# Optimization experiments

Hardware: AMD Instinct MI355X
Metric: run time of the kernel (lower is better)

The kernel has to match this reference:

```python
import jax, jax.numpy as jnp
import numpy as np

N, F, D, H = 8192, 128, 128, 2
LEAKY_ALPHA = 0.3  # keras.layers.LeakyReLU default


def setup_inputs() -> dict:
    key = jax.random.key(0)
    ks = jax.random.split(key, 8)
    x = jax.random.normal(ks[0], (N, F), dtype=jnp.float32)
    # sparse-ish binary adjacency with self loops, stored dense (as the module does)
    adj = (jax.random.uniform(ks[1], (N, N)) < 0.01).astype(jnp.float32)
    adj = jnp.clip(adj + jnp.eye(N, dtype=jnp.float32), 0.0, 1.0)
    s = 1.0 / np.sqrt(F)
    Wmap = jax.random.normal(ks[2], (H, F, D), dtype=jnp.float32) * s
    a1_w = jax.random.normal(ks[3], (H, D), dtype=jnp.float32) * (1.0 / np.sqrt(D))
    a2_w = jax.random.normal(ks[4], (H, D), dtype=jnp.float32) * (1.0 / np.sqrt(D))
    a1_b = jnp.zeros((H,), dtype=jnp.float32)
    a2_b = jnp.zeros((H,), dtype=jnp.float32)
    kernel = jax.random.normal(ks[5], (H, F, D), dtype=jnp.float32) * s
    bias = jnp.zeros((H, N, D), dtype=jnp.float32)
    return {"x": x, "adj": adj, "Wmap": Wmap, "a1_w": a1_w, "a1_b": a1_b,
            "a2_w": a2_w, "a2_b": a2_b, "kernel": kernel, "bias": bias}


def reference(x, adj, Wmap, a1_w, a1_b, a2_w, a2_b, kernel, bias):
    # per-head Conv1D(k=1, no bias): node-wise linear map  [H, N, D]
    mapped = jnp.einsum('nf,hfd->hnd', x, Wmap)
    # per-head Conv1D(k=1) scalar scores  [H, N]
    sa1 = jnp.einsum('hnd,hd->hn', mapped, a1_w) + a1_b[:, None]
    sa2 = jnp.einsum('hnd,hd->hn', mapped, a2_w) + a2_b[:, None]
    # additive score masked multiplicatively by adjacency:  [H, N, N]
    w = adj[None, :, :] * sa1[:, :, None] + adj[None, :, :] * sa2[:, None, :]
    w = jnp.where(w >= 0, w, LEAKY_ALPHA * w)
    att = jax.nn.softmax(w, axis=-1)  # softmax over neighbors (incl. zeroed entries, as in source)
    value = jnp.einsum('nf,hfd->hnd', x, kernel)
    out = jnp.einsum('hnm,hmd->hnd', att, value) + bias  # [H, N, D]
    return out.mean(axis=0)  # attn_heads_reduction='average', linear activation
```

## Files before the change

### kernel.cpp

```cpp
#include <hip/hip_runtime.h>
#include <hip/hip_bf16.h>

#define NN 8192
#define FF 128
#define DD 128
#define HH 2
#define ALPHA 0.3f
#define MAXNNZ 1024

__global__ __launch_bounds__(256) void c_kernel(
    const float* __restrict__ Wmap, const float* __restrict__ a1w,
    const float* __restrict__ a2w, float* __restrict__ c1, float* __restrict__ c2) {
  int t = threadIdx.x;
  int h = t >> 7, f = t & 127;
  const float* wrow = Wmap + ((size_t)h * FF + f) * DD;
  const float* a1 = a1w + h * DD;
  const float* a2 = a2w + h * DD;
  float s1 = 0.f, s2 = 0.f;
  #pragma unroll 8
  for (int d = 0; d < DD; d++) {
    float w = wrow[d];
    s1 += w * a1[d];
    s2 += w * a2[d];
  }
  c1[t] = s1;
  c2[t] = s2;
}

__global__ __launch_bounds__(128) void sa_kernel(
    const float* __restrict__ x, const float* __restrict__ c1,
    const float* __restrict__ c2, const float* __restrict__ a1b,
    const float* __restrict__ a2b, float* __restrict__ sa1, float* __restrict__ sa2) {
  int n = blockIdx.x;
  int f = threadIdx.x;
  float xv = x[(size_t)n * FF + f];
  float p00 = xv * c1[f];
  float p01 = xv * c1[FF + f];
  float p10 = xv * c2[f];
  float p11 = xv * c2[FF + f];
  #pragma unroll
  for (int o = 32; o > 0; o >>= 1) {
    p00 += __shfl_down(p00, o);
    p01 += __shfl_down(p01, o);
    p10 += __shfl_down(p10, o);
    p11 += __shfl_down(p11, o);
  }
  __shared__ float part[2][4];
  int w = f >> 6;
  if ((f & 63) == 0) {
    part[w][0] = p00; part[w][1] = p01; part[w][2] = p10; part[w][3] = p11;
  }
  __syncthreads();
  if (f == 0) {
    sa1[n]      = part[0][0] + part[1][0] + a1b[0];
    sa1[NN + n] = part[0][1] + part[1][1] + a1b[1];
    sa2[n]      = part[0][2] + part[1][2] + a2b[0];
    sa2[NN + n] = part[0][3] + part[1][3] + a2b[1];
  }
}

__global__ __launch_bounds__(256) void value_gemm(
    const float* __restrict__ x, const float* __restrict__ kern,
    float* __restrict__ value) {
  int h = blockIdx.y;
  int row0 = blockIdx.x * 32;
  __shared__ float Bl[64 * 128];
  __shared__ float Al[32 * 129];
  const float4* Bg4 = (const float4*)(kern + (size_t)h * FF * DD);
  const float4* Ag4 = (const float4*)(x + (size_t)row0 * FF);
  float4* Bl4 = (float4*)Bl;
  int tid = threadIdx.x;

  #pragma unroll
  for (int q = 0; q < 4; q++) {
    int idx = q * 256 + tid;
    int r = idx >> 5, c4 = idx & 31;
    float4 g = Ag4[idx];
    Al[r * 129 + c4 * 4 + 0] = g.x;
    Al[r * 129 + c4 * 4 + 1] = g.y;
    Al[r * 129 + c4 * 4 + 2] = g.z;
    Al[r * 129 + c4 * 4 + 3] = g.w;
  }

  int cg = tid & 31;
  int rg = tid >> 5;
  float4 acc[4];
  #pragma unroll
  for (int m = 0; m < 4; m++) acc[m] = make_float4(0.f, 0.f, 0.f, 0.f);

  for (int kp = 0; kp < 2; kp++) {
    __syncthreads();
    #pragma unroll
    for (int q = 0; q < 8; q++)
      Bl4[q * 256 + tid] = Bg4[kp * 2048 + q * 256 + tid];
    __syncthreads();
    for (int k2 = 0; k2 < 64; k2++) {
      int k = kp * 64 + k2;
      float4 bv = *(const float4*)&Bl[k2 * 128 + cg * 4];
      #pragma unroll
      for (int m = 0; m < 4; m++) {
        float av = Al[(rg + m * 8) * 129 + k];
        acc[m].x += av * bv.x;
        acc[m].y += av * bv.y;
        acc[m].z += av * bv.z;
        acc[m].w += av * bv.w;
      }
    }
  }
  #pragma unroll
  for (int m = 0; m < 4; m++) {
    int r = row0 + rg + m * 8;
    *(float4*)&value[((size_t)h * NN + r) * DD + cg * 4] = acc[m];
  }
}

__global__ __launch_bounds__(128) void colsum_kernel(
    const float* __restrict__ value, float* __restrict__ colsum) {
  int h = blockIdx.y, chunk = blockIdx.x, d = threadIdx.x;
  const float* v = value + ((size_t)h * NN + (size_t)chunk * 128) * DD;
  float s = 0.f;
  #pragma unroll 4
  for (int r = 0; r < 128; r++) s += v[r * DD + d];
  atomicAdd(&colsum[h * DD + d], s);
}

__global__ __launch_bounds__(256) void gat_main(
    const float* __restrict__ adj, const float* __restrict__ sa1,
    const float* __restrict__ sa2, const float* __restrict__ value,
    const float* __restrict__ colsum, const float* __restrict__ bias,
    float* __restrict__ out) {
  int i = blockIdx.x;
  __shared__ int idxbuf[MAXNNZ];
  __shared__ float em1buf[HH][MAXNNZ];
  __shared__ int cnt;
  __shared__ float sume_sh[HH];
  __shared__ float wred[4][HH];
  __shared__ float contrib[256];
  int t = threadIdx.x;
  if (t == 0) cnt = 0;
  __syncthreads();

  const float4* arow = (const float4*)(adj + (size_t)i * NN);
  #pragma unroll
  for (int q = 0; q < 8; q++) {
    int f4 = q * 256 + t;
    float4 a = arow[f4];
    int j0 = f4 * 4;
    if (a.x != 0.f) { int p = atomicAdd(&cnt, 1); if (p < MAXNNZ) idxbuf[p] = j0; }
    if (a.y != 0.f) { int p = atomicAdd(&cnt, 1); if (p < MAXNNZ) idxbuf[p] = j0 + 1; }
    if (a.z != 0.f) { int p = atomicAdd(&cnt, 1); if (p < MAXNNZ) idxbuf[p] = j0 + 2; }
    if (a.w != 0.f) { int p = atomicAdd(&cnt, 1); if (p < MAXNNZ) idxbuf[p] = j0 + 3; }
  }
  __syncthreads();
  int count = min(cnt, MAXNNZ);

  float s10 = sa1[i];
  float s11 = sa1[NN + i];
  float l0 = 0.f, l1 = 0.f;
  for (int k = t; k < count; k += 256) {
    int j = idxbuf[k];
    float w0 = s10 + sa2[j];
    float w1 = s11 + sa2[NN + j];
    w0 = (w0 >= 0.f) ? w0 : ALPHA * w0;
    w1 = (w1 >= 0.f) ? w1 : ALPHA * w1;
    float e0 = __expf(w0) - 1.f;
    float e1 = __expf(w1) - 1.f;
    em1buf[0][k] = e0;
    em1buf[1][k] = e1;
    l0 += e0;
    l1 += e1;
  }
  #pragma unroll
  for (int o = 32; o > 0; o >>= 1) {
    l0 += __shfl_down(l0, o);
    l1 += __shfl_down(l1, o);
  }
  int wid = t >> 6;
  if ((t & 63) == 0) { wred[wid][0] = l0; wred[wid][1] = l1; }
  __syncthreads();
  if (t == 0) {
    sume_sh[0] = wred[0][0] + wred[1][0] + wred[2][0] + wred[3][0];
    sume_sh[1] = wred[0][1] + wred[1][1] + wred[2][1] + wred[3][1];
  }
  __syncthreads();

  int h = t >> 7, d = t & 127;
  const float* val = value + (size_t)h * NN * DD + d;
  const float* eb = em1buf[h];
  float acc = 0.f;
  #pragma unroll 4
  for (int k = 0; k < count; k++) {
    int j = idxbuf[k];
    acc += eb[k] * val[(size_t)j * DD];
  }
  float denom = (float)NN + sume_sh[h];
  float r = (colsum[h * DD + d] + acc) / denom +
            bias[((size_t)h * NN + i) * DD + d];
  contrib[t] = r;
  __syncthreads();
  if (t < 128) out[(size_t)i * DD + t] = 0.5f * (contrib[t] + contrib[t + 128]);
}

extern "C" void kernel_launch(void* const* d_in, const int* in_sizes, int n_in,
                              void* d_out, int out_size, void* d_ws, size_t ws_size,
                              hipStream_t stream) {
  const float* x    = (const float*)d_in[0];
  const float* adj  = (const float*)d_in[1];
  const float* Wmap = (const float*)d_in[2];
  const float* a1w  = (const float*)d_in[3];
  const float* a1b  = (const float*)d_in[4];
  const float* a2w  = (const float*)d_in[5];
  const float* a2b  = (const float*)d_in[6];
  const float* kern = (const float*)d_in[7];
  const float* bias = (const float*)d_in[8];
  float* out = (float*)d_out;
  float* ws  = (float*)d_ws;

  float* c1     = ws;
  float* c2     = ws + 256;
  float* sa1    = ws + 512;
  float* sa2    = ws + 16896;
  float* colsum = ws + 33280;
  float* value  = ws + 33536;

  hipMemsetAsync(colsum, 0, HH * DD * sizeof(float), stream);
  c_kernel<<<1, 256, 0, stream>>>(Wmap, a1w, a2w, c1, c2);
  sa_kernel<<<NN, 128, 0, stream>>>(x, c1, c2, a1b, a2b, sa1, sa2);
  value_gemm<<<dim3(NN / 32, HH), 256, 0, stream>>>(x, kern, value);
  colsum_kernel<<<dim3(NN / 128, HH), 128, 0, stream>>>(value, colsum);
  gat_main<<<NN, 256, 0, stream>>>(adj, sa1, sa2, value, colsum, bias, out);
}
```

Measured before the change: 455.4 us.

## Store value in bf16, fuse colsum into GEMM, wave-aggregate neighbor compaction

The value matrix is now stored as bf16, which halves the bytes of the gathered neighbor rows read in the main attention kernel. The column-sum kernel is removed and its work folded into the GEMM epilogue through a shared-memory reduction and atomics. Neighbor index compaction uses one wave-level ballot plus a single atomic per wave instead of one atomic per nonzero. The output store is vectorized to float2. bf16 values lower the accuracy of the weighted sum, while colsum is still accumulated from the fp32 results.

After: 468.1 us. +2.8%, slower.

```diff
diff --git a/kernel.cpp b/kernel.cpp
--- a/kernel.cpp
+++ b/kernel.cpp
@@ -61,7 +61,7 @@
 
 __global__ __launch_bounds__(256) void value_gemm(
     const float* __restrict__ x, const float* __restrict__ kern,
-    float* __restrict__ value) {
+    unsigned short* __restrict__ value_bf, float* __restrict__ colsum) {
   int h = blockIdx.y;
   int row0 = blockIdx.x * 32;
   __shared__ float Bl[64 * 128];
@@ -107,26 +107,46 @@
       }
     }
   }
+
   #pragma unroll
   for (int m = 0; m < 4; m++) {
     int r = row0 + rg + m * 8;
-    *(float4*)&value[((size_t)h * NN + r) * DD + cg * 4] = acc[m];
-  }
-}
-
-__global__ __launch_bounds__(128) void colsum_kernel(
-    const float* __restrict__ value, float* __restrict__ colsum) {
-  int h = blockIdx.y, chunk = blockIdx.x, d = threadIdx.x;
-  const float* v = value + ((size_t)h * NN + (size_t)chunk * 128) * DD;
-  float s = 0.f;
-  #pragma unroll 4
-  for (int r = 0; r < 128; r++) s += v[r * DD + d];
-  atomicAdd(&colsum[h * DD + d], s);
+    ushort4 pk;
+    __hip_bfloat16 b0 = __float2bfloat16(acc[m].x);
+    __hip_bfloat16 b1 = __float2bfloat16(acc[m].y);
+    __hip_bfloat16 b2 = __float2bfloat16(acc[m].z);
+    __hip_bfloat16 b3 = __float2bfloat16(acc[m].w);
+    pk.x = *(unsigned short*)&b0;
+    pk.y = *(unsigned short*)&b1;
+    pk.z = *(unsigned short*)&b2;
+    pk.w = *(unsigned short*)&b3;
+    *(ushort4*)&value_bf[((size_t)h * NN + r) * DD + cg * 4] = pk;
+  }
+
+  float4 cp;
+  cp.x = acc[0].x + acc[1].x + acc[2].x + acc[3].x;
+  cp.y = acc[0].y + acc[1].y + acc[2].y + acc[3].y;
+  cp.z = acc[0].z + acc[1].z + acc[2].z + acc[3].z;
+  cp.w = acc[0].w + acc[1].w + acc[2].w + acc[3].w;
+  __syncthreads();
+  float* colred = Al;
+  *(float4*)&colred[rg * 128 + cg * 4] = cp;
+  __syncthreads();
+  if (rg == 0) {
+    #pragma unroll
+    for (int c = 0; c < 4; c++) {
+      int col = cg * 4 + c;
+      float s = 0.f;
+      #pragma unroll
+      for (int rr = 0; rr < 8; rr++) s += colred[rr * 128 + col];
+      atomicAdd(&colsum[h * DD + col], s);
+    }
+  }
 }
 
 __global__ __launch_bounds__(256) void gat_main(
     const float* __restrict__ adj, const float* __restrict__ sa1,
-    const float* __restrict__ sa2, const float* __restrict__ value,
+    const float* __restrict__ sa2, const unsigned short* __restrict__ value_bf,
     const float* __restrict__ colsum, const float* __restrict__ bias,
     float* __restrict__ out) {
   int i = blockIdx.x;
@@ -137,6 +157,7 @@
   __shared__ float wred[4][HH];
   __shared__ float contrib[256];
   int t = threadIdx.x;
+  int lane = t & 63;
   if (t == 0) cnt = 0;
   __syncthreads();
 
@@ -146,10 +167,20 @@
     int f4 = q * 256 + t;
     float4 a = arow[f4];
     int j0 = f4 * 4;
-    if (a.x != 0.f) { int p = atomicAdd(&cnt, 1); if (p < MAXNNZ) idxbuf[p] = j0; }
-    if (a.y != 0.f) { int p = atomicAdd(&cnt, 1); if (p < MAXNNZ) idxbuf[p] = j0 + 1; }
-    if (a.z != 0.f) { int p = atomicAdd(&cnt, 1); if (p < MAXNNZ) idxbuf[p] = j0 + 2; }
-    if (a.w != 0.f) { int p = atomicAdd(&cnt, 1); if (p < MAXNNZ) idxbuf[p] = j0 + 3; }
+    float av[4] = {a.x, a.y, a.z, a.w};
+    #pragma unroll
+    for (int c = 0; c < 4; c++) {
+      bool nz = (av[c] != 0.f);
+      unsigned long long m = __ballot(nz);
+      int tot = __popcll(m);
+      int base = 0;
+      if (lane == 0 && tot) base = atomicAdd(&cnt, tot);
+      base = __shfl(base, 0);
+      if (nz) {
+        int p = base + __popcll(m & ((1ull << lane) - 1ull));
+        if (p < MAXNNZ) idxbuf[p] = j0 + c;
+      }
+    }
   }
   __syncthreads();
   int count = min(cnt, MAXNNZ);
@@ -176,7 +207,7 @@
     l1 += __shfl_down(l1, o);
   }
   int wid = t >> 6;
-  if ((t & 63) == 0) { wred[wid][0] = l0; wred[wid][1] = l1; }
+  if (lane == 0) { wred[wid][0] = l0; wred[wid][1] = l1; }
   __syncthreads();
   if (t == 0) {
     sume_sh[0] = wred[0][0] + wred[1][0] + wred[2][0] + wred[3][0];
@@ -185,20 +216,27 @@
   __syncthreads();
 
   int h = t >> 7, d = t & 127;
-  const float* val = value + (size_t)h * NN * DD + d;
+  const unsigned short* val = value_bf + (size_t)h * NN * DD + d;
   const float* eb = em1buf[h];
   float acc = 0.f;
   #pragma unroll 4
   for (int k = 0; k < count; k++) {
     int j = idxbuf[k];
-    acc += eb[k] * val[(size_t)j * DD];
+    unsigned short u = val[(size_t)j * DD];
+    __hip_bfloat16 bv = *(__hip_bfloat16*)&u;
+    acc += eb[k] * __bfloat162float(bv);
   }
   float denom = (float)NN + sume_sh[h];
   float r = (colsum[h * DD + d] + acc) / denom +
             bias[((size_t)h * NN + i) * DD + d];
   contrib[t] = r;
   __syncthreads();
-  if (t < 128) out[(size_t)i * DD + t] = 0.5f * (contrib[t] + contrib[t + 128]);
+  if (t < 64) {
+    float2 o2;
+    o2.x = 0.5f * (contrib[2 * t]     + contrib[2 * t + 128]);
+    o2.y = 0.5f * (contrib[2 * t + 1] + contrib[2 * t + 129]);
+    *(float2*)&out[(size_t)i * DD + 2 * t] = o2;
+  }
 }
 
 extern "C" void kernel_launch(void* const* d_in, const int* in_sizes, int n_in,
@@ -221,12 +259,11 @@
   float* sa1    = ws + 512;
   float* sa2    = ws + 16896;
   float* colsum = ws + 33280;
-  float* value  = ws + 33536;
+  unsigned short* value_bf = (unsigned short*)(ws + 33536);
 
   hipMemsetAsync(colsum, 0, HH * DD * sizeof(float), stream);
   c_kernel<<<1, 256, 0, stream>>>(Wmap, a1w, a2w, c1, c2);
   sa_kernel<<<NN, 128, 0, stream>>>(x, c1, c2, a1b, a2b, sa1, sa2);
-  value_gemm<<<dim3(NN / 32, HH), 256, 0, stream>>>(x, kern, value);
-  colsum_kernel<<<dim3(NN / 128, HH), 128, 0, stream>>>(value, colsum);
-  gat_main<<<NN, 256, 0, stream>>>(adj, sa1, sa2, value, colsum, bias, out);
-}
+  value_gemm<<<dim3(NN / 32, HH), 256, 0, stream>>>(x, kern, value_bf, colsum);
+  gat_main<<<NN, 256, 0, stream>>>(adj, sa1, sa2, value_bf, colsum, bias, out);
+}
```
